# Kernel optimization log

Measured on AMD Instinct MI355X. Metric: run time of the kernel, lower is better.

## Reference

```python
import jax, jax.numpy as jnp
import numpy as np

N, L, M, P = 2048, 4096, 512, 512


def setup_inputs() -> dict:
    key = jax.random.key(0)
    ks = jax.random.split(key, 14)
    std = 0.01
    x = jax.random.normal(ks[0], (1, N), dtype=jnp.float32)
    u = jax.random.normal(ks[1], (1, M), dtype=jnp.float32)
    C1 = std * jax.random.normal(ks[2], (L, N), dtype=jnp.float32)
    # D11 is strictly lower triangular (torch: -tril(H22, diagonal=-1))
    D11 = jnp.tril(std * jax.random.normal(ks[3], (L, L), dtype=jnp.float32), -1)
    D12 = std * jax.random.normal(ks[4], (L, M), dtype=jnp.float32)
    # Lambda = 0.5*diag(H22) is positive; keep it bounded away from 0
    Lambda = 0.5 + jax.random.uniform(ks[5], (L,), dtype=jnp.float32)
    F_mat = std * jax.random.normal(ks[6], (N, N), dtype=jnp.float32)
    B1 = std * jax.random.normal(ks[7], (N, L), dtype=jnp.float32)
    B2 = std * jax.random.normal(ks[8], (N, M), dtype=jnp.float32)
    # E must be invertible (it is E = 0.5*(H11 + P_cal + Y - Y^T), PD in practice)
    E = jnp.eye(N, dtype=jnp.float32) + std * jax.random.normal(ks[9], (N, N), dtype=jnp.float32)
    C2 = std * jax.random.normal(ks[10], (P, N), dtype=jnp.float32)
    D21 = std * jax.random.normal(ks[11], (P, L), dtype=jnp.float32)
    D22 = std * jax.random.normal(ks[12], (P, M), dtype=jnp.float32)
    bv = jnp.zeros((L,), dtype=jnp.float32)
    bx = jnp.zeros((N,), dtype=jnp.float32)
    bu = jnp.zeros((P,), dtype=jnp.float32)
    return {"x": x, "u": u, "C1": C1, "D11": D11, "D12": D12, "Lambda": Lambda,
            "F_mat": F_mat, "B1": B1, "B2": B2, "E": E, "C2": C2, "D21": D21,
            "D22": D22, "bv": bv, "bx": bx, "bu": bu, "t": 3}


def reference(x, u, C1, D11, D12, Lambda, F_mat, B1, B2, E, C2, D21, D22, bv, bx, bu, t):
    decay = jnp.float32(0.95) ** t
    # precompute the epsilon-independent part of v for all l rows: (L,)
    a = (x @ C1.T + u @ D12.T)[0] + decay * bv

    # triangular tanh forward substitution: eps[i] = tanh((a[i] + D11[i,:i] @ eps[:i]) / Lambda[i])
    # D11 is strictly lower triangular and eps[j]=0 for j>=i, so a full dot is exact.
    def step(eps, xs):
        i, row, a_i, lam_i = xs
        eps = eps.at[i].set(jnp.tanh((a_i + row @ eps) / lam_i))
        return eps, None

    eps0 = jnp.zeros((L,), dtype=x.dtype)
    eps, _ = jax.lax.scan(step, eps0, (jnp.arange(L), D11, a, Lambda))

    # E x_+ = F x + B1 eps + B2 u + decay*bx  ->  x_+ = (E x_+) E^{-T}
    E_x_ = x @ F_mat.T + eps @ B1.T + u @ B2.T + decay * bx          # (1, N)
    x_ = E_x_ @ jnp.linalg.inv(E).T                                    # (1, N)
    y = x @ C2.T + eps @ D21.T + u @ D22.T + decay * bu                # (1, P)
    return (y, x_)
```

## Files before the change

### kernel.cpp

```cpp
#include <hip/hip_runtime.h>

#define NN 2048
#define LL 4096
#define MM 512
#define PP 512

#define NBLOCKS 256
#define NTHREADS 512
#define SWEEPS 13
#define RICH 10

typedef unsigned short ushort_t;
typedef unsigned int   uint_t;
typedef unsigned long long ull_t;

__device__ __forceinline__ float wave_reduce_sum(float v) {
#pragma unroll
    for (int off = 32; off > 0; off >>= 1) v += __shfl_xor(v, off, 64);
    return v;
}

__device__ __forceinline__ ushort_t f2bf(float f) {
    uint_t x = __float_as_uint(f);
    uint_t r = ((x >> 16) & 1u) + 0x7fffu;
    return (ushort_t)((x + r) >> 16);
}
__device__ __forceinline__ uint_t pack2(float lo, float hi) {
    return (uint_t)f2bf(lo) | ((uint_t)f2bf(hi) << 16);
}
__device__ __forceinline__ float bflo(uint_t w) { return __uint_as_float(w << 16); }
__device__ __forceinline__ float bfhi(uint_t w) { return __uint_as_float(w & 0xffff0000u); }
__device__ __forceinline__ int swz(int j) { return j ^ ((j >> 3) & 7); }

__device__ __forceinline__ uint4 cvt8(float4 f0, float4 f1) {
    uint4 o;
    o.x = pack2(f0.x, f0.y); o.y = pack2(f0.z, f0.w);
    o.z = pack2(f1.x, f1.y); o.w = pack2(f1.z, f1.w);
    return o;
}
__device__ __forceinline__ float dot8(uint4 w, float4 e0, float4 e1, float acc) {
    acc = fmaf(bflo(w.x), e0.x, acc); acc = fmaf(bfhi(w.x), e0.y, acc);
    acc = fmaf(bflo(w.y), e0.z, acc); acc = fmaf(bfhi(w.y), e0.w, acc);
    acc = fmaf(bflo(w.z), e1.x, acc); acc = fmaf(bfhi(w.z), e1.y, acc);
    acc = fmaf(bflo(w.w), e1.z, acc); acc = fmaf(bfhi(w.w), e1.w, acc);
    return acc;
}

__device__ __forceinline__ void tstore(float2* p, float v, int tag) {
    ull_t pk = (ull_t)__float_as_uint(v) | ((ull_t)(uint_t)tag << 32);
    __hip_atomic_store((ull_t*)p, pk, __ATOMIC_RELAXED, __HIP_MEMORY_SCOPE_AGENT);
}

template<int NENT>
__device__ __forceinline__ void stage_vec(const float2* buf, int want,
                                          float* ev, int tid) {
    constexpr int K = NENT / 512;
    const ull_t* p = reinterpret_cast<const ull_t*>(buf);
    ull_t u[K];
    for (;;) {
        int tmin = 0x7fffffff;
#pragma unroll
        for (int k = 0; k < K; ++k) {
            u[k] = __hip_atomic_load(p + tid + k * 512, __ATOMIC_RELAXED,
                                     __HIP_MEMORY_SCOPE_AGENT);
            tmin = min(tmin, (int)(u[k] >> 32));
        }
        if (tmin >= want) break;
        __builtin_amdgcn_s_sleep(1);
    }
#pragma unroll
    for (int k = 0; k < K; ++k) {
        int e = tid + k * 512;
        ev[(swz(e >> 2) << 2) | (e & 3)] = __uint_as_float((uint_t)u[k]);
    }
}

struct KArgs {
    const float *x, *u, *C1, *D11, *D12, *Lam, *F, *B1, *B2, *E, *C2, *D21, *D22;
    const float *bv, *bx, *bu;
    const int* t;
    float* yout; float* xout;
    float2 *epsA, *epsB, *bT, *xaT, *xbT;
};

__global__ __launch_bounds__(512) void clear_tags(ull_t* p) {
    p[blockIdx.x * 512 + threadIdx.x] = 0ull;
}

__device__ __forceinline__ float dot_f32(const float* __restrict__ Mrow,
                                         const float* __restrict__ v,
                                         int n, int lane) {
    const float4* Mr = reinterpret_cast<const float4*>(Mrow);
    const float4* V  = reinterpret_cast<const float4*>(v);
    float acc = 0.f;
    int nv = n >> 2;
    for (int c = lane; c < nv; c += 64) {
        float4 m = Mr[c], vv = V[c];
        acc = fmaf(m.x, vv.x, acc); acc = fmaf(m.y, vv.y, acc);
        acc = fmaf(m.z, vv.z, acc); acc = fmaf(m.w, vv.w, acc);
    }
    return acc;
}

__device__ __forceinline__ float dot_lds_f32(const float* __restrict__ Mrow,
                                             const float4* evec, int nf4, int lane) {
    const float4* Mr = reinterpret_cast<const float4*>(Mrow);
    float acc = 0.f;
    for (int c = lane; c < nf4; c += 64) {
        float4 m = Mr[c];
        float4 e = evec[swz(c)];
        acc = fmaf(m.x, e.x, acc); acc = fmaf(m.y, e.y, acc);
        acc = fmaf(m.z, e.z, acc); acc = fmaf(m.w, e.w, acc);
    }
    return acc;
}

__global__ __launch_bounds__(NTHREADS, 2) void fused_kernel(KArgs A) {
    const int tid  = threadIdx.x;
    const int lane = tid & 63;
    const int warp = tid >> 6;
    const int W    = blockIdx.x * 8 + warp;
    const int rowA = W;
    const int rowB = (LL - 1) - W;

    __shared__ float4 evec[1024];
    float* ev = reinterpret_cast<float*>(evec);

    const float decay = __powf(0.95f, (float)(*A.t));

    float aA, lamA, aB, lamB;
    {
        float acc = dot_f32(A.C1 + (size_t)rowA * NN, A.x, NN, lane)
                  + dot_f32(A.D12 + (size_t)rowA * MM, A.u, MM, lane);
        acc = wave_reduce_sum(acc);
        lamA = A.Lam[rowA];
        aA = fmaf(decay, A.bv[rowA], acc);
        if (lane == 0) tstore(&A.epsA[rowA], tanhf(aA / lamA), 1);

        acc = dot_f32(A.C1 + (size_t)rowB * NN, A.x, NN, lane)
            + dot_f32(A.D12 + (size_t)rowB * MM, A.u, MM, lane);
        acc = wave_reduce_sum(acc);
        lamB = A.Lam[rowB];
        aB = fmaf(decay, A.bv[rowB], acc);
        if (lane == 0) tstore(&A.epsA[rowB], tanhf(aB / lamB), 1);
    }

    float q_r, y0_r = 0.f;
    {
        float acc = dot_f32(A.F + (size_t)W * NN, A.x, NN, lane)
                  + dot_f32(A.B2 + (size_t)W * MM, A.u, MM, lane);
        acc = wave_reduce_sum(acc);
        q_r = fmaf(decay, A.bx[W], acc);
    }
    if (W < PP) {
        float acc = dot_f32(A.C2 + (size_t)W * NN, A.x, NN, lane)
                  + dot_f32(A.D22 + (size_t)W * MM, A.u, MM, lane);
        acc = wave_reduce_sum(acc);
        y0_r = fmaf(decay, A.bu[W], acc);
    }

    uint4 ra[4], rb[8], gr[4];
    {
        const int nhA = (rowA + 7) >> 3;
        const int nhB = (rowB + 7) >> 3;
        const float4* DrA = reinterpret_cast<const float4*>(A.D11 + (size_t)rowA * LL);
        const float4* DrB = reinterpret_cast<const float4*>(A.D11 + (size_t)rowB * LL);
        const float4* Er  = reinterpret_cast<const float4*>(A.E  + (size_t)W * NN);
#pragma unroll
        for (int kk = 0; kk < 4; ++kk) {
            int c = kk * 64 + lane;
            ra[kk] = make_uint4(0u, 0u, 0u, 0u);
            if (c < nhA) ra[kk] = cvt8(DrA[2 * c], DrA[2 * c + 1]);
        }
#pragma unroll
        for (int kk = 0; kk < 8; ++kk) {
            int c = kk * 64 + lane;
            rb[kk] = make_uint4(0u, 0u, 0u, 0u);
            if (c < nhB) rb[kk] = cvt8(DrB[2 * c], DrB[2 * c + 1]);
        }
#pragma unroll
        for (int kk = 0; kk < 4; ++kk) {
            int c = kk * 64 + lane;
            float4 f0 = Er[2 * c], f1 = Er[2 * c + 1];
            int g0 = 8 * c;
            float e[8] = {f0.x, f0.y, f0.z, f0.w, f1.x, f1.y, f1.z, f1.w};
            uint_t wd[4];
#pragma unroll
            for (int j2 = 0; j2 < 4; ++j2) {
                float glo = ((g0 + 2 * j2)     == W ? 1.f : 0.f) - e[2 * j2];
                float ghi = ((g0 + 2 * j2 + 1) == W ? 1.f : 0.f) - e[2 * j2 + 1];
                wd[j2] = pack2(glo, ghi);
            }
            gr[kk] = make_uint4(wd[0], wd[1], wd[2], wd[3]);
        }
    }

    for (int s = 1; s <= SWEEPS; ++s) {
        const float2* in = (s & 1) ? A.epsA : A.epsB;
        float2*      out = (s & 1) ? A.epsB : A.epsA;
        stage_vec<LL>(in, s, ev, tid);
        __syncthreads();
        float sA = 0.f, sB = 0.f;
#pragma unroll
        for (int kk = 0; kk < 4; ++kk) {
            int c = kk * 64 + lane;
            float4 e0 = evec[swz(2 * c)], e1 = evec[swz(2 * c + 1)];
            sA = dot8(ra[kk], e0, e1, sA);
            sB = dot8(rb[kk], e0, e1, sB);
        }
#pragma unroll
        for (int kk = 4; kk < 8; ++kk) {
            int c = kk * 64 + lane;
            float4 e0 = evec[swz(2 * c)], e1 = evec[swz(2 * c + 1)];
            sB = dot8(rb[kk], e0, e1, sB);
        }
        sA = wave_reduce_sum(sA);
        sB = wave_reduce_sum(sB);
        if (lane == 0) {
            tstore(&out[rowA], tanhf((aA + sA) / lamA), s + 1);
            tstore(&out[rowB], tanhf((aB + sB) / lamB), s + 1);
        }
        __syncthreads();
    }

    float b_r;
    {
        const float2* efin = (SWEEPS & 1) ? A.epsB : A.epsA;
        stage_vec<LL>(efin, SWEEPS + 1, ev, tid);
        __syncthreads();
        float acc = dot_lds_f32(A.B1 + (size_t)W * LL, evec, 1024, lane);
        acc = wave_reduce_sum(acc);
        b_r = q_r + acc;
        if (lane == 0) tstore(&A.bT[W], b_r, 1);
        if (W < PP) {
            float ya = dot_lds_f32(A.D21 + (size_t)W * LL, evec, 1024, lane);
            ya = wave_reduce_sum(ya);
            if (lane == 0) A.yout[W] = y0_r + ya;
        }
        __syncthreads();
    }

    {
        float2* buf[2] = { A.xaT, A.xbT };
        for (int k = 0; k < RICH; ++k) {
            const float2* xin = (k == 0) ? A.bT : buf[(k - 1) & 1];
            stage_vec<NN>(xin, k + 1, ev, tid);
            __syncthreads();
            float acc = 0.f;
#pragma unroll
            for (int kk = 0; kk < 4; ++kk) {
                int c = kk * 64 + lane;
                float4 e0 = evec[swz(2 * c)], e1 = evec[swz(2 * c + 1)];
                acc = dot8(gr[kk], e0, e1, acc);
            }
            acc = wave_reduce_sum(acc);
            float val = b_r + acc;
            if (lane == 0) {
                if (k == RICH - 1) A.xout[W] = val;
                else tstore(&buf[k & 1][W], val, k + 2);
            }
            __syncthreads();
        }
    }
}

extern "C" void kernel_launch(void* const* d_in, const int* in_sizes, int n_in,
                              void* d_out, int out_size, void* d_ws, size_t ws_size,
                              hipStream_t stream) {
    KArgs A;
    A.x   = (const float*)d_in[0];
    A.u   = (const float*)d_in[1];
    A.C1  = (const float*)d_in[2];
    A.D11 = (const float*)d_in[3];
    A.D12 = (const float*)d_in[4];
    A.Lam = (const float*)d_in[5];
    A.F   = (const float*)d_in[6];
    A.B1  = (const float*)d_in[7];
    A.B2  = (const float*)d_in[8];
    A.E   = (const float*)d_in[9];
    A.C2  = (const float*)d_in[10];
    A.D21 = (const float*)d_in[11];
    A.D22 = (const float*)d_in[12];
    A.bv  = (const float*)d_in[13];
    A.bx  = (const float*)d_in[14];
    A.bu  = (const float*)d_in[15];
    A.t   = (const int*)d_in[16];
    A.yout = (float*)d_out;
    A.xout = (float*)d_out + PP;

    float2* f2 = (float2*)d_ws;
    A.epsA = f2;
    A.epsB = f2 + 4096;
    A.bT   = f2 + 8192;
    A.xaT  = f2 + 10240;
    A.xbT  = f2 + 12288;

    clear_tags<<<28, 512, 0, stream>>>((ull_t*)d_ws);

    void* params[] = { &A };
    hipLaunchCooperativeKernel((const void*)fused_kernel, dim3(NBLOCKS),
                               dim3(NTHREADS), params, 0, stream);
}
```

Baseline: 150.3 us.

## Preload B1/D21 rows as bf16 registers and batch all prologue loads

Caches x and u in registers and rewrites the initial GEMV dots with fully unrolled, batched loads. The D11 triangular loads become unconditional, and B1 and D21 rows are prefetched into bf16 registers before the sweep loop. The aim is to hide the latency of the post-sweep B1/D21 reads behind the sweeps and raise memory-level parallelism in the prologue. In exchange it raises register pressure a lot (two extra 8x uint4 arrays) at 2 blocks per CU, which risks spills. It also lowers B1/D21 products to bf16 precision.

```diff
diff --git a/kernel.cpp b/kernel.cpp
--- a/kernel.cpp
+++ b/kernel.cpp
@@ -75,6 +75,35 @@
     }
 }
 
+__device__ __forceinline__ float dotN2048(const float* __restrict__ Mrow,
+                                          const float4 (&xr)[8], int lane) {
+    const float4* Mr = reinterpret_cast<const float4*>(Mrow);
+    float4 m[8];
+#pragma unroll
+    for (int k = 0; k < 8; ++k) m[k] = Mr[lane + 64 * k];
+    float acc = 0.f;
+#pragma unroll
+    for (int k = 0; k < 8; ++k) {
+        acc = fmaf(m[k].x, xr[k].x, acc); acc = fmaf(m[k].y, xr[k].y, acc);
+        acc = fmaf(m[k].z, xr[k].z, acc); acc = fmaf(m[k].w, xr[k].w, acc);
+    }
+    return acc;
+}
+__device__ __forceinline__ float dotM512(const float* __restrict__ Mrow,
+                                         const float4 (&ur)[2], int lane) {
+    const float4* Mr = reinterpret_cast<const float4*>(Mrow);
+    float4 m[2];
+#pragma unroll
+    for (int k = 0; k < 2; ++k) m[k] = Mr[lane + 64 * k];
+    float acc = 0.f;
+#pragma unroll
+    for (int k = 0; k < 2; ++k) {
+        acc = fmaf(m[k].x, ur[k].x, acc); acc = fmaf(m[k].y, ur[k].y, acc);
+        acc = fmaf(m[k].z, ur[k].z, acc); acc = fmaf(m[k].w, ur[k].w, acc);
+    }
+    return acc;
+}
+
 struct KArgs {
     const float *x, *u, *C1, *D11, *D12, *Lam, *F, *B1, *B2, *E, *C2, *D21, *D22;
     const float *bv, *bx, *bu;
@@ -87,34 +116,6 @@
     p[blockIdx.x * 512 + threadIdx.x] = 0ull;
 }
 
-__device__ __forceinline__ float dot_f32(const float* __restrict__ Mrow,
-                                         const float* __restrict__ v,
-                                         int n, int lane) {
-    const float4* Mr = reinterpret_cast<const float4*>(Mrow);
-    const float4* V  = reinterpret_cast<const float4*>(v);
-    float acc = 0.f;
-    int nv = n >> 2;
-    for (int c = lane; c < nv; c += 64) {
-        float4 m = Mr[c], vv = V[c];
-        acc = fmaf(m.x, vv.x, acc); acc = fmaf(m.y, vv.y, acc);
-        acc = fmaf(m.z, vv.z, acc); acc = fmaf(m.w, vv.w, acc);
-    }
-    return acc;
-}
-
-__device__ __forceinline__ float dot_lds_f32(const float* __restrict__ Mrow,
-                                             const float4* evec, int nf4, int lane) {
-    const float4* Mr = reinterpret_cast<const float4*>(Mrow);
-    float acc = 0.f;
-    for (int c = lane; c < nf4; c += 64) {
-        float4 m = Mr[c];
-        float4 e = evec[swz(c)];
-        acc = fmaf(m.x, e.x, acc); acc = fmaf(m.y, e.y, acc);
-        acc = fmaf(m.z, e.z, acc); acc = fmaf(m.w, e.w, acc);
-    }
-    return acc;
-}
-
 __global__ __launch_bounds__(NTHREADS, 2) void fused_kernel(KArgs A) {
     const int tid  = threadIdx.x;
     const int lane = tid & 63;
@@ -128,17 +129,27 @@
 
     const float decay = __powf(0.95f, (float)(*A.t));
 
+    float4 xr[8], ur[2];
+    {
+        const float4* Xv = reinterpret_cast<const float4*>(A.x);
+        const float4* Uv = reinterpret_cast<const float4*>(A.u);
+#pragma unroll
+        for (int k = 0; k < 8; ++k) xr[k] = Xv[lane + 64 * k];
+#pragma unroll
+        for (int k = 0; k < 2; ++k) ur[k] = Uv[lane + 64 * k];
+    }
+
     float aA, lamA, aB, lamB;
     {
-        float acc = dot_f32(A.C1 + (size_t)rowA * NN, A.x, NN, lane)
-                  + dot_f32(A.D12 + (size_t)rowA * MM, A.u, MM, lane);
+        float acc = dotN2048(A.C1 + (size_t)rowA * NN, xr, lane)
+                  + dotM512(A.D12 + (size_t)rowA * MM, ur, lane);
         acc = wave_reduce_sum(acc);
         lamA = A.Lam[rowA];
         aA = fmaf(decay, A.bv[rowA], acc);
         if (lane == 0) tstore(&A.epsA[rowA], tanhf(aA / lamA), 1);
 
-        acc = dot_f32(A.C1 + (size_t)rowB * NN, A.x, NN, lane)
-            + dot_f32(A.D12 + (size_t)rowB * MM, A.u, MM, lane);
+        acc = dotN2048(A.C1 + (size_t)rowB * NN, xr, lane)
+            + dotM512(A.D12 + (size_t)rowB * MM, ur, lane);
         acc = wave_reduce_sum(acc);
         lamB = A.Lam[rowB];
         aB = fmaf(decay, A.bv[rowB], acc);
@@ -147,43 +158,54 @@
 
     float q_r, y0_r = 0.f;
     {
-        float acc = dot_f32(A.F + (size_t)W * NN, A.x, NN, lane)
-                  + dot_f32(A.B2 + (size_t)W * MM, A.u, MM, lane);
+        float acc = dotN2048(A.F + (size_t)W * NN, xr, lane)
+                  + dotM512(A.B2 + (size_t)W * MM, ur, lane);
         acc = wave_reduce_sum(acc);
         q_r = fmaf(decay, A.bx[W], acc);
     }
     if (W < PP) {
-        float acc = dot_f32(A.C2 + (size_t)W * NN, A.x, NN, lane)
-                  + dot_f32(A.D22 + (size_t)W * MM, A.u, MM, lane);
+        float acc = dotN2048(A.C2 + (size_t)W * NN, xr, lane)
+                  + dotM512(A.D22 + (size_t)W * MM, ur, lane);
         acc = wave_reduce_sum(acc);
         y0_r = fmaf(decay, A.bu[W], acc);
     }
 
-    uint4 ra[4], rb[8], gr[4];
-    {
-        const int nhA = (rowA + 7) >> 3;
-        const int nhB = (rowB + 7) >> 3;
+    uint4 ra[4], rb[8], gr[4], rb1[8], rd21[8];
+    {
         const float4* DrA = reinterpret_cast<const float4*>(A.D11 + (size_t)rowA * LL);
+        float4 f[8];
+#pragma unroll
+        for (int kk = 0; kk < 4; ++kk) {
+            f[2 * kk]     = DrA[128 * kk + 2 * lane];
+            f[2 * kk + 1] = DrA[128 * kk + 2 * lane + 1];
+        }
+#pragma unroll
+        for (int kk = 0; kk < 4; ++kk) ra[kk] = cvt8(f[2 * kk], f[2 * kk + 1]);
+    }
+    {
         const float4* DrB = reinterpret_cast<const float4*>(A.D11 + (size_t)rowB * LL);
-        const float4* Er  = reinterpret_cast<const float4*>(A.E  + (size_t)W * NN);
+        float4 f[16];
+#pragma unroll
+        for (int kk = 0; kk < 8; ++kk) {
+            f[2 * kk]     = DrB[128 * kk + 2 * lane];
+            f[2 * kk + 1] = DrB[128 * kk + 2 * lane + 1];
+        }
+#pragma unroll
+        for (int kk = 0; kk < 8; ++kk) rb[kk] = cvt8(f[2 * kk], f[2 * kk + 1]);
+    }
+    {
+        const float4* Er = reinterpret_cast<const float4*>(A.E + (size_t)W * NN);
+        float4 f[8];
 #pragma unroll
         for (int kk = 0; kk < 4; ++kk) {
-            int c = kk * 64 + lane;
-            ra[kk] = make_uint4(0u, 0u, 0u, 0u);
-            if (c < nhA) ra[kk] = cvt8(DrA[2 * c], DrA[2 * c + 1]);
-        }
-#pragma unroll
-        for (int kk = 0; kk < 8; ++kk) {
-            int c = kk * 64 + lane;
-            rb[kk] = make_uint4(0u, 0u, 0u, 0u);
-            if (c < nhB) rb[kk] = cvt8(DrB[2 * c], DrB[2 * c + 1]);
+            f[2 * kk]     = Er[128 * kk + 2 * lane];
+            f[2 * kk + 1] = Er[128 * kk + 2 * lane + 1];
         }
 #pragma unroll
         for (int kk = 0; kk < 4; ++kk) {
-            int c = kk * 64 + lane;
-            float4 f0 = Er[2 * c], f1 = Er[2 * c + 1];
-            int g0 = 8 * c;
-            float e[8] = {f0.x, f0.y, f0.z, f0.w, f1.x, f1.y, f1.z, f1.w};
+            int g0 = 8 * (kk * 64 + lane);
+            float e[8] = {f[2*kk].x, f[2*kk].y, f[2*kk].z, f[2*kk].w,
+                          f[2*kk+1].x, f[2*kk+1].y, f[2*kk+1].z, f[2*kk+1].w};
             uint_t wd[4];
 #pragma unroll
             for (int j2 = 0; j2 < 4; ++j2) {
@@ -194,6 +216,31 @@
             gr[kk] = make_uint4(wd[0], wd[1], wd[2], wd[3]);
         }
     }
+    {
+        const float4* Bv = reinterpret_cast<const float4*>(A.B1 + (size_t)W * LL);
+        float4 f[16];
+#pragma unroll
+        for (int kk = 0; kk < 8; ++kk) {
+            f[2 * kk]     = Bv[128 * kk + 2 * lane];
+            f[2 * kk + 1] = Bv[128 * kk + 2 * lane + 1];
+        }
+#pragma unroll
+        for (int kk = 0; kk < 8; ++kk) rb1[kk] = cvt8(f[2 * kk], f[2 * kk + 1]);
+    }
+    if (W < PP) {
+        const float4* Dv = reinterpret_cast<const float4*>(A.D21 + (size_t)W * LL);
+        float4 f[16];
+#pragma unroll
+        for (int kk = 0; kk < 8; ++kk) {
+            f[2 * kk]     = Dv[128 * kk + 2 * lane];
+            f[2 * kk + 1] = Dv[128 * kk + 2 * lane + 1];
+        }
+#pragma unroll
+        for (int kk = 0; kk < 8; ++kk) rd21[kk] = cvt8(f[2 * kk], f[2 * kk + 1]);
+    } else {
+#pragma unroll
+        for (int kk = 0; kk < 8; ++kk) rd21[kk] = make_uint4(0u, 0u, 0u, 0u);
+    }
 
     for (int s = 1; s <= SWEEPS; ++s) {
         const float2* in = (s & 1) ? A.epsA : A.epsB;
@@ -228,14 +275,26 @@
         const float2* efin = (SWEEPS & 1) ? A.epsB : A.epsA;
         stage_vec<LL>(efin, SWEEPS + 1, ev, tid);
         __syncthreads();
-        float acc = dot_lds_f32(A.B1 + (size_t)W * LL, evec, 1024, lane);
-        acc = wave_reduce_sum(acc);
-        b_r = q_r + acc;
+        float accb = 0.f;
+#pragma unroll
+        for (int kk = 0; kk < 8; ++kk) {
+            int c = kk * 64 + lane;
+            float4 e0 = evec[swz(2 * c)], e1 = evec[swz(2 * c + 1)];
+            accb = dot8(rb1[kk], e0, e1, accb);
+        }
+        accb = wave_reduce_sum(accb);
+        b_r = q_r + accb;
         if (lane == 0) tstore(&A.bT[W], b_r, 1);
         if (W < PP) {
-            float ya = dot_lds_f32(A.D21 + (size_t)W * LL, evec, 1024, lane);
-            ya = wave_reduce_sum(ya);
-            if (lane == 0) A.yout[W] = y0_r + ya;
+            float accy = 0.f;
+#pragma unroll
+            for (int kk = 0; kk < 8; ++kk) {
+                int c = kk * 64 + lane;
+                float4 e0 = evec[swz(2 * c)], e1 = evec[swz(2 * c + 1)];
+                accy = dot8(rd21[kk], e0, e1, accy);
+            }
+            accy = wave_reduce_sum(accy);
+            if (lane == 0) A.yout[W] = y0_r + accy;
         }
         __syncthreads();
     }
```

After: 177.0 us. +17.7%, slower.

## Use 1024-thread blocks with one D11 row per wave and early-exit half

Applied to the files above, without the earlier changes.

Blocks grow from 8 to 16 waves, so each wave owns a single D11 row instead of a balanced pair of rows (W and L-1-W). The sweep loop skips chunks beyond the row's triangular length. After the sweeps, the upper half of the blocks exits and the rest handle the N-row B1/D21 and Richardson stages. This raises parallelism per sweep and halves per-wave work, but it loses the load balancing of row pairing, so the waves holding long rows set the critical path. Barriers also span twice as many waves, and the early return relies on staged data that is still written by all blocks.

```diff
diff --git a/kernel.cpp b/kernel.cpp
--- a/kernel.cpp
+++ b/kernel.cpp
@@ -6,7 +6,8 @@
 #define PP 512
 
 #define NBLOCKS 256
-#define NTHREADS 512
+#define NTHREADS 1024
+#define WPB 16
 #define SWEEPS 13
 #define RICH 10
 
@@ -54,14 +55,14 @@
 template<int NENT>
 __device__ __forceinline__ void stage_vec(const float2* buf, int want,
                                           float* ev, int tid) {
-    constexpr int K = NENT / 512;
+    constexpr int K = NENT / NTHREADS;
     const ull_t* p = reinterpret_cast<const ull_t*>(buf);
     ull_t u[K];
     for (;;) {
         int tmin = 0x7fffffff;
 #pragma unroll
         for (int k = 0; k < K; ++k) {
-            u[k] = __hip_atomic_load(p + tid + k * 512, __ATOMIC_RELAXED,
+            u[k] = __hip_atomic_load(p + tid + k * NTHREADS, __ATOMIC_RELAXED,
                                      __HIP_MEMORY_SCOPE_AGENT);
             tmin = min(tmin, (int)(u[k] >> 32));
         }
@@ -70,7 +71,7 @@
     }
 #pragma unroll
     for (int k = 0; k < K; ++k) {
-        int e = tid + k * 512;
+        int e = tid + k * NTHREADS;
         ev[(swz(e >> 2) << 2) | (e & 3)] = __uint_as_float((uint_t)u[k]);
     }
 }
@@ -115,38 +116,29 @@
     return acc;
 }
 
-__global__ __launch_bounds__(NTHREADS, 2) void fused_kernel(KArgs A) {
+__global__ __launch_bounds__(NTHREADS, 4) void fused_kernel(KArgs A) {
     const int tid  = threadIdx.x;
     const int lane = tid & 63;
     const int warp = tid >> 6;
-    const int W    = blockIdx.x * 8 + warp;
-    const int rowA = W;
-    const int rowB = (LL - 1) - W;
+    const int W    = blockIdx.x * WPB + warp;
 
     __shared__ float4 evec[1024];
     float* ev = reinterpret_cast<float*>(evec);
 
     const float decay = __powf(0.95f, (float)(*A.t));
 
-    float aA, lamA, aB, lamB;
+    float a_r, lam_r;
     {
-        float acc = dot_f32(A.C1 + (size_t)rowA * NN, A.x, NN, lane)
-                  + dot_f32(A.D12 + (size_t)rowA * MM, A.u, MM, lane);
-        acc = wave_reduce_sum(acc);
-        lamA = A.Lam[rowA];
-        aA = fmaf(decay, A.bv[rowA], acc);
-        if (lane == 0) tstore(&A.epsA[rowA], tanhf(aA / lamA), 1);
-
-        acc = dot_f32(A.C1 + (size_t)rowB * NN, A.x, NN, lane)
-            + dot_f32(A.D12 + (size_t)rowB * MM, A.u, MM, lane);
-        acc = wave_reduce_sum(acc);
-        lamB = A.Lam[rowB];
-        aB = fmaf(decay, A.bv[rowB], acc);
-        if (lane == 0) tstore(&A.epsA[rowB], tanhf(aB / lamB), 1);
-    }
-
-    float q_r, y0_r = 0.f;
-    {
+        float acc = dot_f32(A.C1 + (size_t)W * NN, A.x, NN, lane)
+                  + dot_f32(A.D12 + (size_t)W * MM, A.u, MM, lane);
+        acc = wave_reduce_sum(acc);
+        lam_r = A.Lam[W];
+        a_r = fmaf(decay, A.bv[W], acc);
+        if (lane == 0) tstore(&A.epsA[W], tanhf(a_r / lam_r), 1);
+    }
+
+    float q_r = 0.f, y0_r = 0.f;
+    if (W < NN) {
         float acc = dot_f32(A.F + (size_t)W * NN, A.x, NN, lane)
                   + dot_f32(A.B2 + (size_t)W * MM, A.u, MM, lane);
         acc = wave_reduce_sum(acc);
@@ -159,25 +151,20 @@
         y0_r = fmaf(decay, A.bu[W], acc);
     }
 
-    uint4 ra[4], rb[8], gr[4];
+    const int nh8   = (W + 7) >> 3;
+    const int kkmax = (nh8 + 63) >> 6;
+    uint4 rd[8], gr[4];
     {
-        const int nhA = (rowA + 7) >> 3;
-        const int nhB = (rowB + 7) >> 3;
-        const float4* DrA = reinterpret_cast<const float4*>(A.D11 + (size_t)rowA * LL);
-        const float4* DrB = reinterpret_cast<const float4*>(A.D11 + (size_t)rowB * LL);
-        const float4* Er  = reinterpret_cast<const float4*>(A.E  + (size_t)W * NN);
-#pragma unroll
-        for (int kk = 0; kk < 4; ++kk) {
-            int c = kk * 64 + lane;
-            ra[kk] = make_uint4(0u, 0u, 0u, 0u);
-            if (c < nhA) ra[kk] = cvt8(DrA[2 * c], DrA[2 * c + 1]);
-        }
+        const float4* Dr = reinterpret_cast<const float4*>(A.D11 + (size_t)W * LL);
 #pragma unroll
         for (int kk = 0; kk < 8; ++kk) {
             int c = kk * 64 + lane;
-            rb[kk] = make_uint4(0u, 0u, 0u, 0u);
-            if (c < nhB) rb[kk] = cvt8(DrB[2 * c], DrB[2 * c + 1]);
-        }
+            rd[kk] = make_uint4(0u, 0u, 0u, 0u);
+            if (c < nh8) rd[kk] = cvt8(Dr[2 * c], Dr[2 * c + 1]);
+        }
+    }
+    if (W < NN) {
+        const float4* Er = reinterpret_cast<const float4*>(A.E + (size_t)W * NN);
 #pragma unroll
         for (int kk = 0; kk < 4; ++kk) {
             int c = kk * 64 + lane;
@@ -193,6 +180,9 @@
             }
             gr[kk] = make_uint4(wd[0], wd[1], wd[2], wd[3]);
         }
+    } else {
+#pragma unroll
+        for (int kk = 0; kk < 4; ++kk) gr[kk] = make_uint4(0u, 0u, 0u, 0u);
     }
 
     for (int s = 1; s <= SWEEPS; ++s) {
@@ -200,28 +190,21 @@
         float2*      out = (s & 1) ? A.epsB : A.epsA;
         stage_vec<LL>(in, s, ev, tid);
         __syncthreads();
-        float sA = 0.f, sB = 0.f;
-#pragma unroll
-        for (int kk = 0; kk < 4; ++kk) {
-            int c = kk * 64 + lane;
-            float4 e0 = evec[swz(2 * c)], e1 = evec[swz(2 * c + 1)];
-            sA = dot8(ra[kk], e0, e1, sA);
-            sB = dot8(rb[kk], e0, e1, sB);
-        }
-#pragma unroll
-        for (int kk = 4; kk < 8; ++kk) {
-            int c = kk * 64 + lane;
-            float4 e0 = evec[swz(2 * c)], e1 = evec[swz(2 * c + 1)];
-            sB = dot8(rb[kk], e0, e1, sB);
-        }
-        sA = wave_reduce_sum(sA);
-        sB = wave_reduce_sum(sB);
-        if (lane == 0) {
-            tstore(&out[rowA], tanhf((aA + sA) / lamA), s + 1);
-            tstore(&out[rowB], tanhf((aB + sB) / lamB), s + 1);
-        }
-        __syncthreads();
-    }
+        float sum = 0.f;
+#pragma unroll
+        for (int kk = 0; kk < 8; ++kk) {
+            if (kk < kkmax) {
+                int c = kk * 64 + lane;
+                float4 e0 = evec[swz(2 * c)], e1 = evec[swz(2 * c + 1)];
+                sum = dot8(rd[kk], e0, e1, sum);
+            }
+        }
+        sum = wave_reduce_sum(sum);
+        if (lane == 0) tstore(&out[W], tanhf((a_r + sum) / lam_r), s + 1);
+        __syncthreads();
+    }
+
+    if (blockIdx.x >= NBLOCKS / 2) return;
 
     float b_r;
     {
@@ -240,27 +223,25 @@
         __syncthreads();
     }
 
-    {
-        float2* buf[2] = { A.xaT, A.xbT };
-        for (int k = 0; k < RICH; ++k) {
-            const float2* xin = (k == 0) ? A.bT : buf[(k - 1) & 1];
-            stage_vec<NN>(xin, k + 1, ev, tid);
-            __syncthreads();
-            float acc = 0.f;
-#pragma unroll
-            for (int kk = 0; kk < 4; ++kk) {
-                int c = kk * 64 + lane;
-                float4 e0 = evec[swz(2 * c)], e1 = evec[swz(2 * c + 1)];
-                acc = dot8(gr[kk], e0, e1, acc);
-            }
-            acc = wave_reduce_sum(acc);
-            float val = b_r + acc;
-            if (lane == 0) {
-                if (k == RICH - 1) A.xout[W] = val;
-                else tstore(&buf[k & 1][W], val, k + 2);
-            }
-            __syncthreads();
-        }
+    for (int k = 0; k < RICH; ++k) {
+        const float2* xin = (k == 0) ? A.bT : ((k & 1) ? A.xaT : A.xbT);
+        float2*       xo  = (k & 1) ? A.xbT : A.xaT;
+        stage_vec<NN>(xin, k + 1, ev, tid);
+        __syncthreads();
+        float acc = 0.f;
+#pragma unroll
+        for (int kk = 0; kk < 4; ++kk) {
+            int c = kk * 64 + lane;
+            float4 e0 = evec[swz(2 * c)], e1 = evec[swz(2 * c + 1)];
+            acc = dot8(gr[kk], e0, e1, acc);
+        }
+        acc = wave_reduce_sum(acc);
+        float val = b_r + acc;
+        if (lane == 0) {
+            if (k == RICH - 1) A.xout[W] = val;
+            else               tstore(&xo[W], val, k + 2);
+        }
+        __syncthreads();
     }
 }
 
```

New measurement: 182.1 us. +21.2%, slower.
